# Kernel tuning notes

Hardware: AMD Instinct MI355X
Metric: run time of the kernel (lower is better)

The kernel has to match this reference:

```python
import jax, jax.numpy as jnp
import numpy as np

N_NODES = 50000
N_EDGES = 800000
X_DIM, H_DIM, Y_DIM = 128, 256, 128


def spmm(adj_vals, adj_row, adj_col, x):
    # sparse [N,N] @ dense [N,D] via gather + segment scatter-add
    msgs = adj_vals[:, None] * x[adj_col]  # [E, D]
    return jax.ops.segment_sum(msgs, adj_row, num_segments=N_NODES)


def setup_inputs() -> dict:
    key = jax.random.key(0)
    ks = jax.random.split(key, 6)
    x = jax.random.uniform(ks[0], (N_NODES, X_DIM), dtype=jnp.float32)
    adj_vals = jax.random.uniform(ks[1], (N_EDGES,), dtype=jnp.float32)
    adj_row = jax.random.randint(ks[2], (N_EDGES,), 0, N_NODES, dtype=jnp.int32)
    adj_col = jax.random.randint(ks[3], (N_EDGES,), 0, N_NODES, dtype=jnp.int32)
    W1 = jax.random.normal(ks[4], (X_DIM, H_DIM), dtype=jnp.float32) * (1.0 / np.sqrt(X_DIM))
    b1 = jnp.zeros((H_DIM,), dtype=jnp.float32)
    W2 = jax.random.normal(ks[5], (H_DIM, Y_DIM), dtype=jnp.float32) * (1.0 / np.sqrt(H_DIM))
    b2 = jnp.zeros((Y_DIM,), dtype=jnp.float32)
    return {"x": x, "adj_vals": adj_vals, "adj_row": adj_row, "adj_col": adj_col,
            "W1": W1, "b1": b1, "W2": W2, "b2": b2}


def reference(x, adj_vals, adj_row, adj_col, W1, b1, W2, b2):
    # row-normalize features: x / (sum_j x_ij + 1e-4)
    x = x / (jnp.sum(x, axis=1, keepdims=True) + 1e-4)
    # layer 1: spmm -> linear -> relu (dropout is identity at eval)
    h = jax.nn.relu(spmm(adj_vals, adj_row, adj_col, x) @ W1 + b1)  # [N, H]
    # layer 2: spmm -> linear
    y = spmm(adj_vals, adj_row, adj_col, h) @ W2 + b2  # [N, Y]
    return y
```

## Files before the change

kernel.cpp:

```cpp
#include <hip/hip_runtime.h>

#define N_NODES 50000
#define N_EDGES 800000
#define X_DIM 128
#define H_DIM 256
#define Y_DIM 128

typedef unsigned int uint32;
typedef unsigned short ushort16;
typedef __attribute__((ext_vector_type(8))) short short8;
typedef __attribute__((ext_vector_type(4))) float floatx4;

__device__ inline ushort16 f2bf(float f) {
    uint32 u = __float_as_uint(f);
    return (ushort16)((u + 0x7FFFu + ((u >> 16) & 1u)) >> 16);
}
__device__ inline float bf_lo(uint32 u) { return __uint_as_float(u << 16); }
__device__ inline float bf_hi(uint32 u) { return __uint_as_float(u & 0xFFFF0000u); }

#define BUCKET_SHIFT 7
#define NB 391
#define CHUNK 4096
#define NCHUNK 196
#define CAP_B 2560

#define NORM_BLOCKS 12500
#define CONV_BLOCKS 256

__global__ __launch_bounds__(256) void prep_kernel(
    const float* __restrict__ x, uint32* __restrict__ xb,
    const float* __restrict__ W1, const float* __restrict__ W2,
    ushort16* __restrict__ W1t, ushort16* __restrict__ W2t,
    const int* __restrict__ rows, int* __restrict__ gpartial) {
    int b = blockIdx.x;
    if (b < NORM_BLOCKS) {
        int row = (b * 256 + threadIdx.x) >> 6;
        int lane = threadIdx.x & 63;
        float2 v = ((const float2*)x)[(size_t)row * 64 + lane];
        float s = v.x + v.y;
        #pragma unroll
        for (int off = 32; off > 0; off >>= 1) s += __shfl_xor(s, off, 64);
        float inv = 1.0f / (s + 1e-4f);
        uint32 lo = (uint32)f2bf(v.x * inv);
        uint32 hi = (uint32)f2bf(v.y * inv);
        xb[(size_t)row * 64 + lane] = lo | (hi << 16);
    } else if (b < NORM_BLOCKS + CONV_BLOCKS) {
        int t = (b - NORM_BLOCKS) * 256 + threadIdx.x;
        if (t < X_DIM * H_DIM) {
            int n = t >> 7, k = t & 127;
            W1t[t] = f2bf(W1[k * H_DIM + n]);
        } else {
            int u = t - X_DIM * H_DIM;
            int y = u >> 8, k = u & 255;
            W2t[u] = f2bf(W2[k * Y_DIM + y]);
        }
    } else {
        __shared__ int h[NB];
        int j = b - NORM_BLOCKS - CONV_BLOCKS;
        int t = threadIdx.x;
        for (int i = t; i < NB; i += 256) h[i] = 0;
        __syncthreads();
        int base = j * CHUNK;
        #pragma unroll
        for (int k = 0; k < CHUNK / 256; k++) {
            int e = base + t + k * 256;
            if (e < N_EDGES) atomicAdd(&h[rows[e] >> BUCKET_SHIFT], 1);
        }
        __syncthreads();
        for (int i = t; i < NB; i += 256) gpartial[j * NB + i] = h[i];
    }
}

__global__ __launch_bounds__(512) void bucket_scan_kernel(
    const int* __restrict__ gpartial, int* __restrict__ bucket_base,
    int* __restrict__ bcursor, int* __restrict__ rowptr) {
    __shared__ int s[512];
    int t = threadIdx.x;
    int total = 0;
    if (t < NB) {
        #pragma unroll 4
        for (int j = 0; j < NCHUNK; j++) total += gpartial[j * NB + t];
    }
    s[t] = total;
    __syncthreads();
    #pragma unroll
    for (int off = 1; off < 512; off <<= 1) {
        int u = (t >= off) ? s[t - off] : 0;
        __syncthreads();
        s[t] += u;
        __syncthreads();
    }
    if (t < NB) {
        int excl = s[t] - total;
        bucket_base[t] = excl;
        bcursor[t] = excl;
    }
    if (t == 0) { bucket_base[NB] = N_EDGES; rowptr[N_NODES] = N_EDGES; }
}

__global__ __launch_bounds__(512) void bucketize_kernel(
    const int* __restrict__ rows, const int* __restrict__ cols,
    const float* __restrict__ vals, const int* __restrict__ gpartial,
    int* __restrict__ bcursor, int2* __restrict__ edges) {
    __shared__ int ob[512];
    __shared__ int c[NB];
    __shared__ int g[NB];
    __shared__ int2 buf[CHUNK];
    int t = threadIdx.x;
    int j = blockIdx.x;
    int base = j * CHUNK;
    int M = N_EDGES - base; if (M > CHUNK) M = CHUNK;
    int cnt = (t < NB) ? gpartial[j * NB + t] : 0;
    ob[t] = cnt;
    __syncthreads();
    #pragma unroll
    for (int off = 1; off < 512; off <<= 1) {
        int u = (t >= off) ? ob[t - off] : 0;
        __syncthreads();
        ob[t] += u;
        __syncthreads();
    }
    ob[t] -= cnt;
    if (t < NB) {
        c[t] = 0;
        g[t] = (cnt > 0) ? atomicAdd(&bcursor[t], cnt) : 0;
    }
    __syncthreads();
    #pragma unroll
    for (int k = 0; k < CHUNK / 512; k++) {
        int e = base + t + k * 512;
        if (e < N_EDGES) {
            int r = rows[e];
            int bb = r >> BUCKET_SHIFT;
            int p = ob[bb] + atomicAdd(&c[bb], 1);
            buf[p] = make_int2(cols[e] | ((r & 127) << 16) | (bb << 23),
                               __float_as_int(vals[e]));
        }
    }
    __syncthreads();
    for (int i = t; i < M; i += 512) {
        int2 e = buf[i];
        int bb = (int)((uint32)e.x >> 23);
        edges[g[bb] + (i - ob[bb])] = e;
    }
}

__global__ __launch_bounds__(256) void bucket_sort_kernel(
    const int* __restrict__ bucket_base, int2* __restrict__ edges,
    int2* __restrict__ scratch, int* __restrict__ rowptr) {
    __shared__ int2 buf[CAP_B];
    __shared__ int2 buf2[CAP_B];
    __shared__ int h[128], o[128], c[128];
    int b = blockIdx.x, t = threadIdx.x;
    int base = bucket_base[b];
    int cnt = bucket_base[b + 1] - base;
    bool fits = (cnt <= CAP_B);
    if (t < 128) h[t] = 0;
    __syncthreads();
    for (int i = t; i < cnt; i += 256) {
        int2 e = edges[base + i];
        if (fits) buf[i] = e; else scratch[base + i] = e;
        atomicAdd(&h[(e.x >> 16) & 127], 1);
    }
    __syncthreads();
    int valh = (t < 128) ? h[t] : 0;
    #pragma unroll
    for (int off = 1; off < 128; off <<= 1) {
        int u = (t >= off && t < 128) ? h[t - off] : 0;
        __syncthreads();
        if (t < 128) h[t] += u;
        __syncthreads();
    }
    if (t < 128) {
        o[t] = h[t] - valh;
        c[t] = 0;
        int i = (b << BUCKET_SHIFT) + t;
        if (i < N_NODES) rowptr[i] = base + h[t] - valh;
    }
    __syncthreads();
    for (int i = t; i < cnt; i += 256) {
        int2 e = fits ? buf[i] : scratch[base + i];
        int lr = (e.x >> 16) & 127;
        int p = o[lr] + atomicAdd(&c[lr], 1);
        if (fits) buf2[p] = e; else edges[base + p] = e;
    }
    __syncthreads();
    if (fits)
        for (int i = t; i < cnt; i += 256) edges[base + i] = buf2[i];
}

template <bool OUT_F32>
__global__ __launch_bounds__(256) void spmm_csr_bf16(
    const uint32* __restrict__ feat, const int* __restrict__ rowptr,
    const int2* __restrict__ edges, const float* __restrict__ bias,
    void* __restrict__ outv) {
    int row = (blockIdx.x * blockDim.x + threadIdx.x) >> 6;
    int lane = threadIdx.x & 63;
    if (row >= N_NODES) return;
    int start = rowptr[row], end = rowptr[row + 1];
    float ax0 = 0.f, ay0 = 0.f, ax1 = 0.f, ay1 = 0.f;
    float ax2 = 0.f, ay2 = 0.f, ax3 = 0.f, ay3 = 0.f;
    for (int base = start; base < end; base += 64) {
        int n = end - base; if (n > 64) n = 64;
        int2 ev = make_int2(0, 0);
        if (lane < n) ev = edges[base + lane];
        int c = ev.x & 0xFFFF; float v = __int_as_float(ev.y);
        int j = 0;
        for (; j + 8 <= n; j += 8) {
            int c0 = __shfl(c, j, 64), c1 = __shfl(c, j + 1, 64);
            int c2 = __shfl(c, j + 2, 64), c3 = __shfl(c, j + 3, 64);
            int c4 = __shfl(c, j + 4, 64), c5 = __shfl(c, j + 5, 64);
            int c6 = __shfl(c, j + 6, 64), c7 = __shfl(c, j + 7, 64);
            float v0 = __shfl(v, j, 64), v1 = __shfl(v, j + 1, 64);
            float v2 = __shfl(v, j + 2, 64), v3 = __shfl(v, j + 3, 64);
            float v4 = __shfl(v, j + 4, 64), v5 = __shfl(v, j + 5, 64);
            float v6 = __shfl(v, j + 6, 64), v7 = __shfl(v, j + 7, 64);
            uint32 f0 = feat[(size_t)c0 * 64 + lane];
            uint32 f1 = feat[(size_t)c1 * 64 + lane];
            uint32 f2 = feat[(size_t)c2 * 64 + lane];
            uint32 f3 = feat[(size_t)c3 * 64 + lane];
            uint32 f4 = feat[(size_t)c4 * 64 + lane];
            uint32 f5 = feat[(size_t)c5 * 64 + lane];
            uint32 f6 = feat[(size_t)c6 * 64 + lane];
            uint32 f7 = feat[(size_t)c7 * 64 + lane];
            ax0 += v0 * bf_lo(f0); ay0 += v0 * bf_hi(f0);
            ax1 += v1 * bf_lo(f1); ay1 += v1 * bf_hi(f1);
            ax2 += v2 * bf_lo(f2); ay2 += v2 * bf_hi(f2);
            ax3 += v3 * bf_lo(f3); ay3 += v3 * bf_hi(f3);
            ax0 += v4 * bf_lo(f4); ay0 += v4 * bf_hi(f4);
            ax1 += v5 * bf_lo(f5); ay1 += v5 * bf_hi(f5);
            ax2 += v6 * bf_lo(f6); ay2 += v6 * bf_hi(f6);
            ax3 += v7 * bf_lo(f7); ay3 += v7 * bf_hi(f7);
        }
        for (; j + 4 <= n; j += 4) {
            int c0 = __shfl(c, j, 64), c1 = __shfl(c, j + 1, 64);
            int c2 = __shfl(c, j + 2, 64), c3 = __shfl(c, j + 3, 64);
            float v0 = __shfl(v, j, 64), v1 = __shfl(v, j + 1, 64);
            float v2 = __shfl(v, j + 2, 64), v3 = __shfl(v, j + 3, 64);
            uint32 f0 = feat[(size_t)c0 * 64 + lane];
            uint32 f1 = feat[(size_t)c1 * 64 + lane];
            uint32 f2 = feat[(size_t)c2 * 64 + lane];
            uint32 f3 = feat[(size_t)c3 * 64 + lane];
            ax0 += v0 * bf_lo(f0); ay0 += v0 * bf_hi(f0);
            ax1 += v1 * bf_lo(f1); ay1 += v1 * bf_hi(f1);
            ax2 += v2 * bf_lo(f2); ay2 += v2 * bf_hi(f2);
            ax3 += v3 * bf_lo(f3); ay3 += v3 * bf_hi(f3);
        }
        for (; j < n; j++) {
            int c0 = __shfl(c, j, 64);
            float v0 = __shfl(v, j, 64);
            uint32 f0 = feat[(size_t)c0 * 64 + lane];
            ax0 += v0 * bf_lo(f0); ay0 += v0 * bf_hi(f0);
        }
    }
    float ax = (ax0 + ax1) + (ax2 + ax3);
    float ay = (ay0 + ay1) + (ay2 + ay3);
    if (OUT_F32) {
        float2 b = ((const float2*)bias)[lane];
        ((float2*)outv)[(size_t)row * 64 + lane] = make_float2(ax + b.x, ay + b.y);
    } else {
        ((uint32*)outv)[(size_t)row * 64 + lane] =
            (uint32)f2bf(ax) | ((uint32)f2bf(ay) << 16);
    }
}

__global__ __launch_bounds__(256, 3) void gemm_fused(
    const uint32* __restrict__ agg1, const ushort16* __restrict__ W1t,
    const ushort16* __restrict__ W2t, const float* __restrict__ b1,
    ushort16* __restrict__ hw, int nrows) {
    __shared__ ushort16 a_s[64 * 136];
    __shared__ ushort16 h_s[64 * 264];
    const int tx = threadIdx.x;
    const int wave = tx >> 6, lane = tx & 63;
    const int quad = lane >> 4, l16 = lane & 15;
    const int row0 = blockIdx.x * 64;

    short8 bfr1[4][4];
    #pragma unroll
    for (int ct = 0; ct < 4; ct++)
        #pragma unroll
        for (int kk = 0; kk < 4; kk++)
            bfr1[ct][kk] = *(const short8*)
                &W1t[(wave * 64 + ct * 16 + l16) * 128 + kk * 32 + quad * 8];

    #pragma unroll
    for (int i = 0; i < 16; i++) {
        int idx = tx + i * 256;
        int r = idx >> 6, c = idx & 63;
        uint32 v = 0;
        if (row0 + r < nrows) v = agg1[(size_t)(row0 + r) * 64 + c];
        *(uint32*)&a_s[r * 136 + c * 2] = v;
    }
    __syncthreads();

    floatx4 acc1[4][4];
    #pragma unroll
    for (int rs = 0; rs < 4; rs++)
        #pragma unroll
        for (int ct = 0; ct < 4; ct++)
            #pragma unroll
            for (int j = 0; j < 4; j++) acc1[rs][ct][j] = 0.f;
    #pragma unroll
    for (int kk = 0; kk < 4; kk++) {
        #pragma unroll
        for (int rs = 0; rs < 4; rs++) {
            short8 af = *(const short8*)&a_s[(rs * 16 + l16) * 136 + kk * 32 + quad * 8];
            #pragma unroll
            for (int ct = 0; ct < 4; ct++)
                acc1[rs][ct] = __builtin_amdgcn_mfma_f32_16x16x32_bf16(
                    af, bfr1[ct][kk], acc1[rs][ct], 0, 0, 0);
        }
    }
    float bv[4];
    #pragma unroll
    for (int ct = 0; ct < 4; ct++) bv[ct] = b1[wave * 64 + ct * 16 + l16];
    #pragma unroll
    for (int rs = 0; rs < 4; rs++)
        #pragma unroll
        for (int ct = 0; ct < 4; ct++)
            #pragma unroll
            for (int reg = 0; reg < 4; reg++) {
                float v = acc1[rs][ct][reg] + bv[ct];
                v = v > 0.f ? v : 0.f;
                h_s[(rs * 16 + quad * 4 + reg) * 264 + wave * 64 + ct * 16 + l16] = f2bf(v);
            }

    short8 bfr2[2][8];
    #pragma unroll
    for (int ct = 0; ct < 2; ct++)
        #pragma unroll
        for (int kk = 0; kk < 8; kk++)
            bfr2[ct][kk] = *(const short8*)
                &W2t[(wave * 32 + ct * 16 + l16) * 256 + kk * 32 + quad * 8];
    __syncthreads();

    floatx4 acc2[4][2];
    #pragma unroll
    for (int rs = 0; rs < 4; rs++)
        #pragma unroll
        for (int ct = 0; ct < 2; ct++)
            #pragma unroll
            for (int j = 0; j < 4; j++) acc2[rs][ct][j] = 0.f;
    #pragma unroll
    for (int kk = 0; kk < 8; kk++) {
        #pragma unroll
        for (int rs = 0; rs < 4; rs++) {
            short8 af = *(const short8*)&h_s[(rs * 16 + l16) * 264 + kk * 32 + quad * 8];
            #pragma unroll
            for (int ct = 0; ct < 2; ct++)
                acc2[rs][ct] = __builtin_amdgcn_mfma_f32_16x16x32_bf16(
                    af, bfr2[ct][kk], acc2[rs][ct], 0, 0, 0);
        }
    }
    #pragma unroll
    for (int rs = 0; rs < 4; rs++)
        #pragma unroll
        for (int ct = 0; ct < 2; ct++)
            #pragma unroll
            for (int reg = 0; reg < 4; reg++) {
                int row = row0 + rs * 16 + quad * 4 + reg;
                if (row < nrows)
                    hw[(size_t)row * 128 + wave * 32 + ct * 16 + l16] =
                        f2bf(acc2[rs][ct][reg]);
            }
}

extern "C" void kernel_launch(void* const* d_in, const int* in_sizes, int n_in,
                              void* d_out, int out_size, void* d_ws, size_t ws_size,
                              hipStream_t stream) {
    const float* x = (const float*)d_in[0];
    const float* adj_vals = (const float*)d_in[1];
    const int* adj_row = (const int*)d_in[2];
    const int* adj_col = (const int*)d_in[3];
    const float* W1 = (const float*)d_in[4];
    const float* b1 = (const float*)d_in[5];
    const float* W2 = (const float*)d_in[6];
    const float* b2 = (const float*)d_in[7];
    float* out = (float*)d_out;

    char* ws = (char*)d_ws;
    uint32*   xb       = (uint32*)  (ws + 0);
    uint32*   agg1     = (uint32*)  (ws + 12800000);
    ushort16* hw       = (ushort16*)(ws + 25600000);
    int2*     edges    = (int2*)    (ws + 38400000);
    int2*     scratch  = (int2*)    (ws + 44800000);
    int*      gpartial = (int*)     (ws + 51200000);
    int*      rowptr   = (int*)     (ws + 51513344);
    int*      bbase    = (int*)     (ws + 51714048);
    int*      bcursor  = (int*)     (ws + 51716096);
    ushort16* W1t      = (ushort16*)(ws + 51718144);
    ushort16* W2t      = (ushort16*)(ws + 51783680);

    hipLaunchKernelGGL(prep_kernel, dim3(NORM_BLOCKS + CONV_BLOCKS + NCHUNK),
                       dim3(256), 0, stream, x, xb, W1, W2, W1t, W2t,
                       adj_row, gpartial);

    hipLaunchKernelGGL(bucket_scan_kernel, dim3(1), dim3(512),
                       0, stream, gpartial, bbase, bcursor, rowptr);

    hipLaunchKernelGGL(bucketize_kernel, dim3(NCHUNK), dim3(512),
                       0, stream, adj_row, adj_col, adj_vals, gpartial, bcursor, edges);
    hipLaunchKernelGGL(bucket_sort_kernel, dim3(NB), dim3(256),
                       0, stream, bbase, edges, scratch, rowptr);

    hipLaunchKernelGGL((spmm_csr_bf16<false>), dim3((N_NODES * 64 + 255) / 256), dim3(256),
                       0, stream, xb, rowptr, edges, (const float*)nullptr, (void*)agg1);

    hipLaunchKernelGGL(gemm_fused, dim3((N_NODES + 63) / 64), dim3(256),
                       0, stream, agg1, W1t, W2t, b1, hw, N_NODES);

    hipLaunchKernelGGL((spmm_csr_bf16<true>), dim3((N_NODES * 64 + 255) / 256), dim3(256),
                       0, stream, (const uint32*)hw, rowptr, edges, b2, (void*)out);
}
```

Before: 223.8 us.

## Fuse first SpMM into the two-layer GEMM kernel and pad gather tails

The first-layer sparse aggregation now runs inside the GEMM kernel. Each of 8 waves aggregates 8 rows straight into shared memory, so the bf16 agg1 buffer is no longer written to and read back from global memory, and one launch is removed. The GEMM work is split across 8 waves of a 512-thread block, so each wave holds fewer weight fragments. The 4-wide and scalar tail loops are replaced by rounding the edge count up to a multiple of 8; padded lanes use column 0 with weight 0, trading a few wasted loads for less branching. The risk is that the sparse gather inside the larger block may suffer from lower occupancy or register pressure under launch_bounds(512,4).

```diff
diff --git a/kernel.cpp b/kernel.cpp
--- a/kernel.cpp
+++ b/kernel.cpp
@@ -189,15 +189,10 @@
         for (int i = t; i < cnt; i += 256) edges[base + i] = buf2[i];
 }
 
-template <bool OUT_F32>
-__global__ __launch_bounds__(256) void spmm_csr_bf16(
-    const uint32* __restrict__ feat, const int* __restrict__ rowptr,
-    const int2* __restrict__ edges, const float* __restrict__ bias,
-    void* __restrict__ outv) {
-    int row = (blockIdx.x * blockDim.x + threadIdx.x) >> 6;
-    int lane = threadIdx.x & 63;
-    if (row >= N_NODES) return;
-    int start = rowptr[row], end = rowptr[row + 1];
+__device__ inline void spmm_row(const uint32* __restrict__ feat,
+                                const int2* __restrict__ edges,
+                                int start, int end, int lane,
+                                float& AX, float& AY) {
     float ax0 = 0.f, ay0 = 0.f, ax1 = 0.f, ay1 = 0.f;
     float ax2 = 0.f, ay2 = 0.f, ax3 = 0.f, ay3 = 0.f;
     for (int base = start; base < end; base += 64) {
@@ -205,8 +200,8 @@
         int2 ev = make_int2(0, 0);
         if (lane < n) ev = edges[base + lane];
         int c = ev.x & 0xFFFF; float v = __int_as_float(ev.y);
-        int j = 0;
-        for (; j + 8 <= n; j += 8) {
+        int n8 = (n + 7) & ~7;
+        for (int j = 0; j < n8; j += 8) {
             int c0 = __shfl(c, j, 64), c1 = __shfl(c, j + 1, 64);
             int c2 = __shfl(c, j + 2, 64), c3 = __shfl(c, j + 3, 64);
             int c4 = __shfl(c, j + 4, 64), c5 = __shfl(c, j + 5, 64);
@@ -232,42 +227,16 @@
             ax2 += v6 * bf_lo(f6); ay2 += v6 * bf_hi(f6);
             ax3 += v7 * bf_lo(f7); ay3 += v7 * bf_hi(f7);
         }
-        for (; j + 4 <= n; j += 4) {
-            int c0 = __shfl(c, j, 64), c1 = __shfl(c, j + 1, 64);
-            int c2 = __shfl(c, j + 2, 64), c3 = __shfl(c, j + 3, 64);
-            float v0 = __shfl(v, j, 64), v1 = __shfl(v, j + 1, 64);
-            float v2 = __shfl(v, j + 2, 64), v3 = __shfl(v, j + 3, 64);
-            uint32 f0 = feat[(size_t)c0 * 64 + lane];
-            uint32 f1 = feat[(size_t)c1 * 64 + lane];
-            uint32 f2 = feat[(size_t)c2 * 64 + lane];
-            uint32 f3 = feat[(size_t)c3 * 64 + lane];
-            ax0 += v0 * bf_lo(f0); ay0 += v0 * bf_hi(f0);
-            ax1 += v1 * bf_lo(f1); ay1 += v1 * bf_hi(f1);
-            ax2 += v2 * bf_lo(f2); ay2 += v2 * bf_hi(f2);
-            ax3 += v3 * bf_lo(f3); ay3 += v3 * bf_hi(f3);
-        }
-        for (; j < n; j++) {
-            int c0 = __shfl(c, j, 64);
-            float v0 = __shfl(v, j, 64);
-            uint32 f0 = feat[(size_t)c0 * 64 + lane];
-            ax0 += v0 * bf_lo(f0); ay0 += v0 * bf_hi(f0);
-        }
-    }
-    float ax = (ax0 + ax1) + (ax2 + ax3);
-    float ay = (ay0 + ay1) + (ay2 + ay3);
-    if (OUT_F32) {
-        float2 b = ((const float2*)bias)[lane];
-        ((float2*)outv)[(size_t)row * 64 + lane] = make_float2(ax + b.x, ay + b.y);
-    } else {
-        ((uint32*)outv)[(size_t)row * 64 + lane] =
-            (uint32)f2bf(ax) | ((uint32)f2bf(ay) << 16);
-    }
-}
-
-__global__ __launch_bounds__(256, 3) void gemm_fused(
-    const uint32* __restrict__ agg1, const ushort16* __restrict__ W1t,
+    }
+    AX = (ax0 + ax1) + (ax2 + ax3);
+    AY = (ay0 + ay1) + (ay2 + ay3);
+}
+
+__global__ __launch_bounds__(512, 4) void spmm_gemm_fused(
+    const uint32* __restrict__ xb, const int* __restrict__ rowptr,
+    const int2* __restrict__ edges, const ushort16* __restrict__ W1t,
     const ushort16* __restrict__ W2t, const float* __restrict__ b1,
-    ushort16* __restrict__ hw, int nrows) {
+    ushort16* __restrict__ hw) {
     __shared__ ushort16 a_s[64 * 136];
     __shared__ ushort16 h_s[64 * 264];
     const int tx = threadIdx.x;
@@ -275,29 +244,33 @@
     const int quad = lane >> 4, l16 = lane & 15;
     const int row0 = blockIdx.x * 64;
 
-    short8 bfr1[4][4];
-    #pragma unroll
-    for (int ct = 0; ct < 4; ct++)
+    short8 bfr1[2][4];
+    #pragma unroll
+    for (int ct = 0; ct < 2; ct++)
         #pragma unroll
         for (int kk = 0; kk < 4; kk++)
             bfr1[ct][kk] = *(const short8*)
-                &W1t[(wave * 64 + ct * 16 + l16) * 128 + kk * 32 + quad * 8];
-
-    #pragma unroll
-    for (int i = 0; i < 16; i++) {
-        int idx = tx + i * 256;
-        int r = idx >> 6, c = idx & 63;
-        uint32 v = 0;
-        if (row0 + r < nrows) v = agg1[(size_t)(row0 + r) * 64 + c];
-        *(uint32*)&a_s[r * 136 + c * 2] = v;
-    }
-    __syncthreads();
-
-    floatx4 acc1[4][4];
+                &W1t[(wave * 32 + ct * 16 + l16) * 128 + kk * 32 + quad * 8];
+
+    #pragma unroll
+    for (int i = 0; i < 8; i++) {
+        int r = wave * 8 + i;
+        int row = row0 + r;
+        float ax = 0.f, ay = 0.f;
+        if (row < N_NODES) {
+            int start = rowptr[row], end = rowptr[row + 1];
+            spmm_row(xb, edges, start, end, lane, ax, ay);
+        }
+        *(uint32*)&a_s[r * 136 + lane * 2] =
+            (uint32)f2bf(ax) | ((uint32)f2bf(ay) << 16);
+    }
+    __syncthreads();
+
+    floatx4 acc1[4][2];
     #pragma unroll
     for (int rs = 0; rs < 4; rs++)
         #pragma unroll
-        for (int ct = 0; ct < 4; ct++)
+        for (int ct = 0; ct < 2; ct++)
             #pragma unroll
             for (int j = 0; j < 4; j++) acc1[rs][ct][j] = 0.f;
     #pragma unroll
@@ -306,63 +279,67 @@
         for (int rs = 0; rs < 4; rs++) {
             short8 af = *(const short8*)&a_s[(rs * 16 + l16) * 136 + kk * 32 + quad * 8];
             #pragma unroll
-            for (int ct = 0; ct < 4; ct++)
+            for (int ct = 0; ct < 2; ct++)
                 acc1[rs][ct] = __builtin_amdgcn_mfma_f32_16x16x32_bf16(
                     af, bfr1[ct][kk], acc1[rs][ct], 0, 0, 0);
         }
     }
-    float bv[4];
-    #pragma unroll
-    for (int ct = 0; ct < 4; ct++) bv[ct] = b1[wave * 64 + ct * 16 + l16];
+    float bv[2];
+    #pragma unroll
+    for (int ct = 0; ct < 2; ct++) bv[ct] = b1[wave * 32 + ct * 16 + l16];
     #pragma unroll
     for (int rs = 0; rs < 4; rs++)
         #pragma unroll
-        for (int ct = 0; ct < 4; ct++)
+        for (int ct = 0; ct < 2; ct++)
             #pragma unroll
             for (int reg = 0; reg < 4; reg++) {
                 float v = acc1[rs][ct][reg] + bv[ct];
                 v = v > 0.f ? v : 0.f;
-                h_s[(rs * 16 + quad * 4 + reg) * 264 + wave * 64 + ct * 16 + l16] = f2bf(v);
+                h_s[(rs * 16 + quad * 4 + reg) * 264 + wave * 32 + ct * 16 + l16] = f2bf(v);
             }
 
-    short8 bfr2[2][8];
-    #pragma unroll
-    for (int ct = 0; ct < 2; ct++)
-        #pragma unroll
-        for (int kk = 0; kk < 8; kk++)
-            bfr2[ct][kk] = *(const short8*)
-                &W2t[(wave * 32 + ct * 16 + l16) * 256 + kk * 32 + quad * 8];
-    __syncthreads();
-
-    floatx4 acc2[4][2];
+    short8 bfr2[8];
+    #pragma unroll
+    for (int kk = 0; kk < 8; kk++)
+        bfr2[kk] = *(const short8*)
+            &W2t[(wave * 16 + l16) * 256 + kk * 32 + quad * 8];
+    __syncthreads();
+
+    floatx4 acc2[4];
     #pragma unroll
     for (int rs = 0; rs < 4; rs++)
         #pragma unroll
-        for (int ct = 0; ct < 2; ct++)
-            #pragma unroll
-            for (int j = 0; j < 4; j++) acc2[rs][ct][j] = 0.f;
+        for (int j = 0; j < 4; j++) acc2[rs][j] = 0.f;
     #pragma unroll
     for (int kk = 0; kk < 8; kk++) {
         #pragma unroll
         for (int rs = 0; rs < 4; rs++) {
             short8 af = *(const short8*)&h_s[(rs * 16 + l16) * 264 + kk * 32 + quad * 8];
-            #pragma unroll
-            for (int ct = 0; ct < 2; ct++)
-                acc2[rs][ct] = __builtin_amdgcn_mfma_f32_16x16x32_bf16(
-                    af, bfr2[ct][kk], acc2[rs][ct], 0, 0, 0);
+            acc2[rs] = __builtin_amdgcn_mfma_f32_16x16x32_bf16(
+                af, bfr2[kk], acc2[rs], 0, 0, 0);
         }
     }
     #pragma unroll
     for (int rs = 0; rs < 4; rs++)
         #pragma unroll
-        for (int ct = 0; ct < 2; ct++)
-            #pragma unroll
-            for (int reg = 0; reg < 4; reg++) {
-                int row = row0 + rs * 16 + quad * 4 + reg;
-                if (row < nrows)
-                    hw[(size_t)row * 128 + wave * 32 + ct * 16 + l16] =
-                        f2bf(acc2[rs][ct][reg]);
-            }
+        for (int reg = 0; reg < 4; reg++) {
+            int row = row0 + rs * 16 + quad * 4 + reg;
+            if (row < N_NODES)
+                hw[(size_t)row * 128 + wave * 16 + l16] = f2bf(acc2[rs][reg]);
+        }
+}
+
+__global__ __launch_bounds__(256) void spmm_out_kernel(
+    const uint32* __restrict__ feat, const int* __restrict__ rowptr,
+    const int2* __restrict__ edges, const float* __restrict__ bias,
+    float* __restrict__ out) {
+    int row = (blockIdx.x * blockDim.x + threadIdx.x) >> 6;
+    int lane = threadIdx.x & 63;
+    if (row >= N_NODES) return;
+    float ax, ay;
+    spmm_row(feat, edges, rowptr[row], rowptr[row + 1], lane, ax, ay);
+    float2 b = ((const float2*)bias)[lane];
+    ((float2*)out)[(size_t)row * 64 + lane] = make_float2(ax + b.x, ay + b.y);
 }
 
 extern "C" void kernel_launch(void* const* d_in, const int* in_sizes, int n_in,
@@ -380,16 +357,15 @@
 
     char* ws = (char*)d_ws;
     uint32*   xb       = (uint32*)  (ws + 0);
-    uint32*   agg1     = (uint32*)  (ws + 12800000);
-    ushort16* hw       = (ushort16*)(ws + 25600000);
-    int2*     edges    = (int2*)    (ws + 38400000);
-    int2*     scratch  = (int2*)    (ws + 44800000);
-    int*      gpartial = (int*)     (ws + 51200000);
-    int*      rowptr   = (int*)     (ws + 51513344);
-    int*      bbase    = (int*)     (ws + 51714048);
-    int*      bcursor  = (int*)     (ws + 51716096);
-    ushort16* W1t      = (ushort16*)(ws + 51718144);
-    ushort16* W2t      = (ushort16*)(ws + 51783680);
+    ushort16* hw       = (ushort16*)(ws + 12800000);
+    int2*     edges    = (int2*)    (ws + 25600000);
+    int2*     scratch  = (int2*)    (ws + 32000000);
+    int*      gpartial = (int*)     (ws + 38400000);
+    int*      rowptr   = (int*)     (ws + 38713344);
+    int*      bbase    = (int*)     (ws + 38914048);
+    int*      bcursor  = (int*)     (ws + 38916096);
+    ushort16* W1t      = (ushort16*)(ws + 38918144);
+    ushort16* W2t      = (ushort16*)(ws + 38983680);
 
     hipLaunchKernelGGL(prep_kernel, dim3(NORM_BLOCKS + CONV_BLOCKS + NCHUNK),
                        dim3(256), 0, stream, x, xb, W1, W2, W1t, W2t,
@@ -403,12 +379,9 @@
     hipLaunchKernelGGL(bucket_sort_kernel, dim3(NB), dim3(256),
                        0, stream, bbase, edges, scratch, rowptr);
 
-    hipLaunchKernelGGL((spmm_csr_bf16<false>), dim3((N_NODES * 64 + 255) / 256), dim3(256),
-                       0, stream, xb, rowptr, edges, (const float*)nullptr, (void*)agg1);
-
-    hipLaunchKernelGGL(gemm_fused, dim3((N_NODES + 63) / 64), dim3(256),
-                       0, stream, agg1, W1t, W2t, b1, hw, N_NODES);
-
-    hipLaunchKernelGGL((spmm_csr_bf16<true>), dim3((N_NODES * 64 + 255) / 256), dim3(256),
-                       0, stream, (const uint32*)hw, rowptr, edges, b2, (void*)out);
-}
+    hipLaunchKernelGGL(spmm_gemm_fused, dim3((N_NODES + 63) / 64), dim3(512),
+                       0, stream, xb, rowptr, edges, W1t, W2t, b1, hw);
+
+    hipLaunchKernelGGL(spmm_out_kernel, dim3((N_NODES * 64 + 255) / 256), dim3(256),
+                       0, stream, (const uint32*)hw, rowptr, edges, b2, out);
+}
```

Result: no change. 223.5 us (-0.1%).
